# Performance work log

Measured on AMD Instinct MI355X. Metric: run time of the kernel, lower is better.

Reference implementation:

```python
import jax, jax.numpy as jnp
import numpy as np

# angular momenta of the full basis (2s,3s,2p,3p,3d) -> block sizes 1,1,3,3,5; norb=13
L_LIST = [0, 0, 1, 1, 2]


def factor_matrix():
    """Replicates the orbital-pair loop: factor 0.5 on diagonal orbital blocks,
    1.0 for i<j blocks, 0.0 below the block diagonal (only i<=j filled)."""
    sizes = [2 * l + 1 for l in L_LIST]
    norb = sum(sizes)
    F = np.zeros((norb, norb), np.float32)
    ist = 0
    for i, si in enumerate(sizes):
        jst = 0
        for j, sj in enumerate(sizes):
            if i < j:
                F[ist:ist + si, jst:jst + sj] = 1.0
            elif i == j:
                F[ist:ist + si, jst:jst + sj] = 0.5
            jst += sj
        ist += si
    return jnp.asarray(F)


def setup_inputs() -> dict:
    key = jax.random.key(0)
    k1, k2, k3, k4, k5 = jax.random.split(key, 5)
    N, E, K = 128, 2048, 16
    norb = sum(2 * l + 1 for l in L_LIST)  # 13
    return {
        "hopping": jax.random.normal(k1, (E, norb * norb), jnp.float32),
        "onsite": jax.random.normal(k2, (N, norb * norb), jnp.float32),
        "kpoints": jax.random.uniform(k3, (K, 3), jnp.float32),
        "cell_shift": jax.random.normal(k4, (E, 3), jnp.float32),
        "edge_index": jax.random.randint(k5, (2, E), 0, N, jnp.int64),
    }


def reference(hopping, onsite, kpoints, cell_shift, edge_index):
    F = factor_matrix()
    norb = F.shape[0]
    N = onsite.shape[0]
    K = kpoints.shape[0]
    ctype = jnp.complex64

    # per-edge / per-atom orbital blocks with upper-triangular factor (i<=j loop)
    hop = (hopping.reshape(-1, norb, norb) * F).astype(ctype)   # [E,norb,norb]
    ons = (onsite.reshape(-1, norb, norb) * F).astype(ctype)    # [N,norb,norb]

    # Bloch phase exp(-i 2*pi k.R) per (k, edge)
    phase = jnp.exp(-1j * 2.0 * jnp.pi * (kpoints @ cell_shift.T).astype(ctype))  # [K,E]

    # assemble block Hamiltonian [K, N, N, norb, norb]
    H = jnp.zeros((K, N, N, norb, norb), ctype)
    ar = jnp.arange(N)
    H = H.at[:, ar, ar].add(ons[None])  # onsite diagonal blocks (no phase)
    ie, je = edge_index[0], edge_index[1]
    H = H.at[:, ie, je].add(phase[:, :, None, None] * hop[None])  # scatter-add edges

    # hermitize: block + block^H (swap atom blocks and orbital indices)
    H = H + jnp.conj(jnp.swapaxes(jnp.swapaxes(H, 1, 2), 3, 4))
    # [K, N, norb, N, norb] -> [K, all_norb, all_norb]
    Hk = H.transpose(0, 1, 3, 2, 4).reshape(K, N * norb, N * norb)
    return Hk
```

## Files before the change

kernel.cpp:

```cpp
#include <hip/hip_runtime.h>
#include <math.h>

#define NORB 13
#define NORB2 (NORB * NORB)
#define GB 16
#define KSPLIT 2

typedef float fx4 __attribute__((ext_vector_type(4)));

__device__ __forceinline__ int blk_of(int p) {
    return p < 1 ? 0 : (p < 2 ? 1 : (p < 5 ? 2 : (p < 8 ? 3 : 4)));
}
__device__ __forceinline__ float ffac(int p, int q) {
    int bp = blk_of(p), bq = blk_of(q);
    return bp < bq ? 1.0f : (bp == bq ? 0.5f : 0.0f);
}

__global__ void __launch_bounds__(256)
k_build(const int* __restrict__ edge_index, int* __restrict__ rowptr,
        int* __restrict__ entries, int E, int N, int ngroups) {
    extern __shared__ int sm[];
    int nbins = N * ngroups;
    int* cnt    = sm;
    int* cursor = sm + nbins;
    int* part   = sm + 2 * nbins;
    int tid = threadIdx.x;

    for (int i = tid; i < nbins; i += 256) cnt[i] = 0;
    __syncthreads();

    for (int e = tid; e < E; e += 256) {
        int ie = edge_index[e], je = edge_index[E + e];
        atomicAdd(cnt + ie * ngroups + (je >> 4), 1);
        atomicAdd(cnt + je * ngroups + (ie >> 4), 1);
    }
    __syncthreads();

    int per = nbins / 256;
    int base = tid * per;
    int s = 0;
    for (int i = 0; i < per; ++i) s += cnt[base + i];
    part[tid + 1] = s;
    __syncthreads();
    if (tid == 0) {
        part[0] = 0;
        for (int i = 1; i <= 256; ++i) part[i] += part[i - 1];
    }
    __syncthreads();
    int run = part[tid];
    for (int i = 0; i < per; ++i) {
        rowptr[base + i] = run;
        cursor[base + i] = run;
        run += cnt[base + i];
    }
    if (tid == 255) rowptr[nbins] = run;
    __syncthreads();

    for (int e = tid; e < E; e += 256) {
        int ie = edge_index[e], je = edge_index[E + e];
        int pos = atomicAdd(cursor + ie * ngroups + (je >> 4), 1);
        entries[pos] = (e << 9) | je;
        pos = atomicAdd(cursor + je * ngroups + (ie >> 4), 1);
        entries[pos] = (e << 9) | 256 | ie;
    }
}

__global__ void __launch_bounds__(256)
k_assemble(const float* __restrict__ hopping,
           const float* __restrict__ onsite,
           const float* __restrict__ kpoints,
           const float* __restrict__ cell_shift,
           const int* __restrict__ rowptr,
           const int* __restrict__ entries,
           float* __restrict__ out,
           int N, int K, int ld, int es, int ngroups) {
    int g  = blockIdx.x % ngroups;
    int a  = (blockIdx.x / ngroups) % N;
    int kc = blockIdx.x / (ngroups * N);
    int kch = (K + KSPLIT - 1) / KSPLIT;
    int k0 = kc * kch, k1 = min(K, k0 + kch);
    int tid = threadIdx.x;
    int b0 = g * GB;
    int nb = min(GB, N - b0);

    __shared__ __align__(16) float lds[NORB * GB * NORB * 2];
    fx4* lds4 = (fx4*)lds;
    const int LDSF4 = NORB * GB * NORB * 2 / 4;
    for (int i = tid; i < LDSF4; i += 256)
        lds4[i] = (fx4){0.f, 0.f, 0.f, 0.f};

    int p = 0, q = 0;
    bool act = tid < NORB2;
    if (act) { p = tid / NORB; q = tid - p * NORB; }
    float fpq = act ? ffac(p, q) : 0.f;
    float fqp = act ? ffac(q, p) : 0.f;

    bool diag = (a >= b0 && a < b0 + nb);
    float onv = 0.f;
    int  ondst = 0;
    if (diag && act) {
        const float* on = onsite + (size_t)a * NORB2;
        onv = on[p * NORB + q] * fpq + on[q * NORB + p] * fqp;
        ondst = (p * GB * NORB + (a - b0) * NORB + q) * 2;
    }

    int bin = a * ngroups + g;
    int beg = rowptr[bin], end = rowptr[bin + 1];
    __syncthreads();

    const int ROWF4 = GB * NORB * 2 / 4;
    bool fastpath = (es == 2) && (nb == GB);

    for (int k = k0; k < k1; ++k) {
        float kx = kpoints[3 * k], ky = kpoints[3 * k + 1], kz = kpoints[3 * k + 2];

        if (diag && act) {
            lds[ondst] += onv;
        }
        for (int it = beg; it < end; ++it) {
            int ent = entries[it];
            int e = ent >> 9;
            int rev = ent & 256;
            int i = (ent & 255) - b0;
            float Rx = cell_shift[3 * e], Ry = cell_shift[3 * e + 1], Rz = cell_shift[3 * e + 2];
            float d = kx * Rx + ky * Ry + kz * Rz;
            float s, c;
            __sincosf(-6.2831853071795864f * d, &s, &c);
            float im = rev ? -s : s;
            if (act) {
                const float* h = hopping + (size_t)e * NORB2;
                float hv = rev ? h[q * NORB + p] * fqp : h[p * NORB + q] * fpq;
                int base = (p * GB * NORB + i * NORB + q) * 2;
                lds[base]     += c * hv;
                lds[base + 1] += im * hv;
            }
        }
        __syncthreads();

        if (fastpath) {
            fx4* o4 = (fx4*)out;
            for (int idx = tid; idx < NORB * ROWF4; idx += 256) {
                int row = idx / ROWF4;
                int col = idx - row * ROWF4;
                fx4 v = lds4[idx];
                lds4[idx] = (fx4){0.f, 0.f, 0.f, 0.f};
                size_t gc = ((size_t)k * ld + (size_t)a * NORB + row) * ld + (size_t)b0 * NORB;
                o4[(gc >> 1) + col] = v;
            }
        } else if (es == 2) {
            float2* o2 = (float2*)out;
            int nelem = NORB * nb * NORB;
            for (int idx = tid; idx < nelem; idx += 256) {
                int row = idx / (nb * NORB);
                int rem = idx - row * nb * NORB;
                size_t gc = ((size_t)k * ld + (size_t)a * NORB + row) * ld + (size_t)b0 * NORB + rem;
                int li = (row * GB * NORB + rem) * 2;
                o2[gc] = make_float2(lds[li], lds[li + 1]);
                lds[li] = 0.f; lds[li + 1] = 0.f;
            }
        } else {
            int nelem = NORB * nb * NORB;
            for (int idx = tid; idx < nelem; idx += 256) {
                int row = idx / (nb * NORB);
                int rem = idx - row * nb * NORB;
                size_t gc = ((size_t)k * ld + (size_t)a * NORB + row) * ld + (size_t)b0 * NORB + rem;
                int li = (row * GB * NORB + rem) * 2;
                out[gc] = lds[li];
                lds[li] = 0.f; lds[li + 1] = 0.f;
            }
        }
        __syncthreads();
    }
}

extern "C" void kernel_launch(void* const* d_in, const int* in_sizes, int n_in,
                              void* d_out, int out_size, void* d_ws, size_t ws_size,
                              hipStream_t stream) {
    const float* hopping    = (const float*)d_in[0];
    const float* onsite     = (const float*)d_in[1];
    const float* kpoints    = (const float*)d_in[2];
    const float* cell_shift = (const float*)d_in[3];
    const int*   edge_index = (const int*)d_in[4];
    float* out = (float*)d_out;

    int E = in_sizes[0] / NORB2;
    int N = in_sizes[1] / NORB2;
    int K = in_sizes[2] / 3;
    int ld = N * NORB;
    int ngroups = (N + GB - 1) / GB;
    int nbins = N * ngroups;

    size_t full = (size_t)K * ld * ld * 2;
    int es = ((size_t)out_size >= full) ? 2 : 1;

    int* rowptr  = (int*)d_ws;
    int* entries = rowptr + nbins + 1;

    size_t build_lds = (size_t)(2 * nbins + 257) * sizeof(int);
    k_build<<<1, 256, build_lds, stream>>>(edge_index, rowptr, entries, E, N, ngroups);

    int nwg = N * ngroups * KSPLIT;
    k_assemble<<<nwg, 256, 0, stream>>>(hopping, onsite, kpoints, cell_shift,
                                        rowptr, entries, out, N, K, ld, es, ngroups);
}
```

Before: 223.8 us.

## Double-buffer LDS strips per k-point and halve column group width

The column group width is halved and the k-point split across workgroups is removed, so each workgroup now walks all k-points for one (atom, column group) pair. The LDS strip is double-buffered so the edge accumulation for k+1 can overlap the global store of strip k, with one barrier per k instead of two. Halving the group width keeps the workgroup count about the same while each store row shrinks to 8 blocks, which makes the stores less contiguous and means each workgroup runs a longer serial k loop.

```diff
diff --git a/kernel.cpp b/kernel.cpp
--- a/kernel.cpp
+++ b/kernel.cpp
@@ -3,8 +3,10 @@
 
 #define NORB 13
 #define NORB2 (NORB * NORB)
-#define GB 16
-#define KSPLIT 2
+#define GB 8
+#define SF (NORB * GB * NORB * 2)
+#define SF4 (SF / 4)
+#define ROWF4 (GB * NORB * 2 / 4)
 
 typedef float fx4 __attribute__((ext_vector_type(4)));
 
@@ -31,8 +33,8 @@
 
     for (int e = tid; e < E; e += 256) {
         int ie = edge_index[e], je = edge_index[E + e];
-        atomicAdd(cnt + ie * ngroups + (je >> 4), 1);
-        atomicAdd(cnt + je * ngroups + (ie >> 4), 1);
+        atomicAdd(cnt + ie * ngroups + je / GB, 1);
+        atomicAdd(cnt + je * ngroups + ie / GB, 1);
     }
     __syncthreads();
 
@@ -58,9 +60,9 @@
 
     for (int e = tid; e < E; e += 256) {
         int ie = edge_index[e], je = edge_index[E + e];
-        int pos = atomicAdd(cursor + ie * ngroups + (je >> 4), 1);
+        int pos = atomicAdd(cursor + ie * ngroups + je / GB, 1);
         entries[pos] = (e << 9) | je;
-        pos = atomicAdd(cursor + je * ngroups + (ie >> 4), 1);
+        pos = atomicAdd(cursor + je * ngroups + ie / GB, 1);
         entries[pos] = (e << 9) | 256 | ie;
     }
 }
@@ -75,18 +77,14 @@
            float* __restrict__ out,
            int N, int K, int ld, int es, int ngroups) {
     int g  = blockIdx.x % ngroups;
-    int a  = (blockIdx.x / ngroups) % N;
-    int kc = blockIdx.x / (ngroups * N);
-    int kch = (K + KSPLIT - 1) / KSPLIT;
-    int k0 = kc * kch, k1 = min(K, k0 + kch);
+    int a  = blockIdx.x / ngroups;
     int tid = threadIdx.x;
     int b0 = g * GB;
     int nb = min(GB, N - b0);
 
-    __shared__ __align__(16) float lds[NORB * GB * NORB * 2];
+    __shared__ __align__(16) float lds[2 * SF];
     fx4* lds4 = (fx4*)lds;
-    const int LDSF4 = NORB * GB * NORB * 2 / 4;
-    for (int i = tid; i < LDSF4; i += 256)
+    for (int i = tid; i < 2 * SF4; i += 256)
         lds4[i] = (fx4){0.f, 0.f, 0.f, 0.f};
 
     int p = 0, q = 0;
@@ -108,15 +106,12 @@
     int beg = rowptr[bin], end = rowptr[bin + 1];
     __syncthreads();
 
-    const int ROWF4 = GB * NORB * 2 / 4;
     bool fastpath = (es == 2) && (nb == GB);
 
-    for (int k = k0; k < k1; ++k) {
+    auto accumulate = [&](int k) {
+        float* B = lds + (k & 1) * SF;
         float kx = kpoints[3 * k], ky = kpoints[3 * k + 1], kz = kpoints[3 * k + 2];
-
-        if (diag && act) {
-            lds[ondst] += onv;
-        }
+        if (diag && act) B[ondst] += onv;
         for (int it = beg; it < end; ++it) {
             int ent = entries[it];
             int e = ent >> 9;
@@ -131,23 +126,26 @@
                 const float* h = hopping + (size_t)e * NORB2;
                 float hv = rev ? h[q * NORB + p] * fqp : h[p * NORB + q] * fpq;
                 int base = (p * GB * NORB + i * NORB + q) * 2;
-                lds[base]     += c * hv;
-                lds[base + 1] += im * hv;
+                B[base]     += c * hv;
+                B[base + 1] += im * hv;
             }
         }
-        __syncthreads();
-
+    };
+
+    auto store_strip = [&](int k) {
         if (fastpath) {
+            fx4* B4 = lds4 + (k & 1) * SF4;
             fx4* o4 = (fx4*)out;
             for (int idx = tid; idx < NORB * ROWF4; idx += 256) {
                 int row = idx / ROWF4;
                 int col = idx - row * ROWF4;
-                fx4 v = lds4[idx];
-                lds4[idx] = (fx4){0.f, 0.f, 0.f, 0.f};
+                fx4 v = B4[idx];
+                B4[idx] = (fx4){0.f, 0.f, 0.f, 0.f};
                 size_t gc = ((size_t)k * ld + (size_t)a * NORB + row) * ld + (size_t)b0 * NORB;
                 o4[(gc >> 1) + col] = v;
             }
         } else if (es == 2) {
+            float* B = lds + (k & 1) * SF;
             float2* o2 = (float2*)out;
             int nelem = NORB * nb * NORB;
             for (int idx = tid; idx < nelem; idx += 256) {
@@ -155,21 +153,28 @@
                 int rem = idx - row * nb * NORB;
                 size_t gc = ((size_t)k * ld + (size_t)a * NORB + row) * ld + (size_t)b0 * NORB + rem;
                 int li = (row * GB * NORB + rem) * 2;
-                o2[gc] = make_float2(lds[li], lds[li + 1]);
-                lds[li] = 0.f; lds[li + 1] = 0.f;
+                o2[gc] = make_float2(B[li], B[li + 1]);
+                B[li] = 0.f; B[li + 1] = 0.f;
             }
         } else {
+            float* B = lds + (k & 1) * SF;
             int nelem = NORB * nb * NORB;
             for (int idx = tid; idx < nelem; idx += 256) {
                 int row = idx / (nb * NORB);
                 int rem = idx - row * nb * NORB;
                 size_t gc = ((size_t)k * ld + (size_t)a * NORB + row) * ld + (size_t)b0 * NORB + rem;
                 int li = (row * GB * NORB + rem) * 2;
-                out[gc] = lds[li];
-                lds[li] = 0.f; lds[li + 1] = 0.f;
+                out[gc] = B[li];
+                B[li] = 0.f; B[li + 1] = 0.f;
             }
         }
+    };
+
+    accumulate(0);
+    for (int k = 0; k < K; ++k) {
         __syncthreads();
+        store_strip(k);
+        if (k + 1 < K) accumulate(k + 1);
     }
 }
 
@@ -199,7 +204,7 @@
     size_t build_lds = (size_t)(2 * nbins + 257) * sizeof(int);
     k_build<<<1, 256, build_lds, stream>>>(edge_index, rowptr, entries, E, N, ngroups);
 
-    int nwg = N * ngroups * KSPLIT;
+    int nwg = N * ngroups;
     k_assemble<<<nwg, 256, 0, stream>>>(hopping, onsite, kpoints, cell_shift,
                                         rowptr, entries, out, N, K, ld, es, ngroups);
 }
```

Result: slower. 233.4 us (+4.3%).
